# Kernel tuning notes

Measured on AMD Instinct MI355X. Metric: run time of the kernel, lower is better.

Reference implementation:

```python
import jax, jax.numpy as jnp
import numpy as np

N, H, V, K = 2048, 1024, 50304, 16
C = V // K  # tokens per POS cluster


def setup_inputs() -> dict:
    key = jax.random.key(0)
    kx, ky, kw, kl = jax.random.split(key, 4)
    x = jax.random.normal(kx, (N, H), dtype=jnp.float32)
    y = jax.random.randint(ky, (N,), 0, V, dtype=jnp.int32)
    # consistent POS label: token y belongs to cluster y // C
    y_pos = (y // C).astype(jnp.int32)
    # pos2token[i] = token ids of cluster i (equal contiguous partition)
    pos2token = jnp.arange(V, dtype=jnp.int32).reshape(K, C)
    # token_in_pos_id[i][v] = within-cluster index of token v in cluster i
    token_in_pos_id = jnp.broadcast_to(jnp.arange(V, dtype=jnp.int32) % C, (K, V))
    cluster_w = jax.random.normal(kw, (H, K), dtype=jnp.float32) * 0.02
    logits = jax.random.normal(kl, (H, V), dtype=jnp.float32) * 0.02
    return {"x": x, "y": y, "y_pos": y_pos, "pos2token": pos2token,
            "token_in_pos_id": token_in_pos_id, "cluster_w": cluster_w, "logits": logits}


def reference(x, y, y_pos, pos2token, token_in_pos_id, cluster_w, logits):
    # cluster (POS) log-probs: [N, K]
    cluster_ll = jax.nn.log_softmax(x @ cluster_w, axis=1)
    # per-cluster weight slices gathered once: [H, K, C]
    W = logits[:, pos2token.reshape(-1)].reshape(H, K, C)
    # tail logits for every token against every cluster's token set: [N, K, C]
    tail_lp = jax.nn.log_softmax(jnp.einsum('nh,hkc->nkc', x, W), axis=-1)
    n = jnp.arange(y.shape[0])
    within = token_in_pos_id[y_pos, y]          # within-cluster target id
    nll = -cluster_ll[n, y_pos] - tail_lp[n, y_pos, within]
    return nll
```

## Files before the change

kernel.cpp:

```cpp
#include <hip/hip_runtime.h>
#include <hip/hip_bf16.h>
#include <stdint.h>

#define NROW 2048
#define HDIM 1024
#define VOC  50304
#define KCL  16
#define CDIM 3144

#define MT 64
#define NT 256
#define BK 32
#define PK 36
#define NCT 13
#define MAXTILES 48

#define WS_SUMEXP 0
#define WS_COUNTS 2048
#define WS_PART   2064
#define WS_ZTGT   4112
#define WS_TCOL   6160
#define WS_ROWS   8208
#define WS_NTILE  40976
#define WS_TILES  40977

typedef unsigned short u16;
typedef __attribute__((ext_vector_type(8))) short short8;
typedef __attribute__((ext_vector_type(4))) short short4v;
typedef __attribute__((ext_vector_type(4))) float f32x4;
typedef __attribute__((ext_vector_type(4))) unsigned short ushort4v;

__device__ __forceinline__ ushort2 f2bf2(float a, float b) {
    union { __hip_bfloat162 h; ushort2 u; } cv;
    cv.h = __float22bfloat162_rn(float2{a, b});
    return cv.u;
}

__global__ void scatter_kernel(const int* __restrict__ y,
                               const int* __restrict__ y_pos,
                               const int* __restrict__ tip,
                               int* ws_i) {
    int n = blockIdx.x * 256 + threadIdx.x;
    if (n >= NROW) return;
    int kn = y_pos[n];
    int slot = atomicAdd(&ws_i[WS_COUNTS + kn], 1);
    ws_i[WS_ROWS + kn * NROW + slot] = n;
    ws_i[WS_TCOL + n] = tip[kn * VOC + y[n]];
}

__global__ void plan_kernel(int* ws_i) {
    int lane = threadIdx.x;
    int nt = (lane < KCL) ? (ws_i[WS_COUNTS + lane] + MT - 1) / MT : 0;
    int pre = nt;
#pragma unroll
    for (int off = 1; off < 16; off <<= 1) {
        int v = __shfl_up(pre, off);
        if ((lane & 15) >= off) pre += v;
    }
    int start = pre - nt;
    if (lane < KCL) {
        for (int r = 0; r < nt; r++) {
            ws_i[WS_TILES + 2 * (start + r)]     = lane;
            ws_i[WS_TILES + 2 * (start + r) + 1] = r;
        }
        if (lane == KCL - 1) ws_i[WS_NTILE] = start + nt;
    }
}

__global__ void cluster_kernel(const float* __restrict__ x,
                               const float* __restrict__ cw,
                               const int* __restrict__ y_pos,
                               float* ws_f) {
    int wave = threadIdx.x >> 6;
    int lane = threadIdx.x & 63;
    int n = blockIdx.x * 4 + wave;
    float acc[KCL];
#pragma unroll
    for (int k = 0; k < KCL; k++) acc[k] = 0.f;
#pragma unroll
    for (int j = 0; j < 16; j++) {
        int h = j * 64 + lane;
        float xv = x[(size_t)n * HDIM + h];
        const float4* cwr = (const float4*)(cw + (size_t)h * KCL);
#pragma unroll
        for (int q = 0; q < 4; q++) {
            float4 w = cwr[q];
            acc[q * 4 + 0] += xv * w.x;
            acc[q * 4 + 1] += xv * w.y;
            acc[q * 4 + 2] += xv * w.z;
            acc[q * 4 + 3] += xv * w.w;
        }
    }
#pragma unroll
    for (int off = 32; off >= 1; off >>= 1) {
#pragma unroll
        for (int k = 0; k < KCL; k++) acc[k] += __shfl_down(acc[k], off);
    }
    if (lane == 0) {
        int kn = y_pos[n];
        float m = acc[0];
#pragma unroll
        for (int k = 1; k < KCL; k++) m = fmaxf(m, acc[k]);
        float s = 0.f, skn = 0.f;
#pragma unroll
        for (int k = 0; k < KCL; k++) {
            s += __expf(acc[k] - m);
            skn = (k == kn) ? acc[k] : skn;
        }
        ws_f[WS_PART + n] = (m + __logf(s)) - skn;
    }
}

__launch_bounds__(256)
__global__ void tail_kernel(const float* __restrict__ x,
                            const float* __restrict__ logits,
                            const int* ws_i, float* ws_f) {
    __shared__ __align__(16) u16 As[MT * PK];
    __shared__ __align__(16) u16 Bs[NT * PK];
    __shared__ int   lrow[MT];
    __shared__ int   ltcol[MT];
    __shared__ float rowsum[MT];

    const int ntile = ws_i[WS_NTILE];
    if ((int)blockIdx.y >= ntile) return;
    const int kcl = ws_i[WS_TILES + 2 * blockIdx.y];
    const int rt  = ws_i[WS_TILES + 2 * blockIdx.y + 1];
    const int ct  = blockIdx.x;
    const int Mk  = ws_i[WS_COUNTS + kcl];

    const int tid = threadIdx.x;
    if (tid < MT) {
        int r = rt * MT + tid;
        int rid = (r < Mk) ? ws_i[WS_ROWS + kcl * NROW + r] : -1;
        lrow[tid]  = rid;
        ltcol[tid] = (rid >= 0) ? ws_i[WS_TCOL + rid] : -1;
        rowsum[tid] = 0.f;
    }
    __syncthreads();

    const int w    = tid >> 6;
    const int l    = tid & 63;
    const int quad = l >> 4;
    const int lm   = l & 15;

    const int arow = tid >> 2;
    const int ak0  = (tid & 3) * 8;
    int rid_s = lrow[arow]; if (rid_s < 0) rid_s = 0;
    const float* ap = x + (size_t)rid_s * HDIM + ak0;
    int gc = ct * NT + tid; if (gc >= CDIM) gc = CDIM - 1;
    const float* bp = logits + (size_t)(kcl * CDIM + gc);

    float ar[8];
    float br[BK];
#pragma unroll
    for (int j = 0; j < 8; j++) ar[j] = ap[j];
#pragma unroll
    for (int k = 0; k < BK; k++) br[k] = bp[(size_t)k * VOC];
    ap += BK;
    bp += (size_t)BK * VOC;

    f32x4 acc[4][4];
#pragma unroll
    for (int mi = 0; mi < 4; mi++)
#pragma unroll
        for (int ni = 0; ni < 4; ni++) acc[mi][ni] = (f32x4)(0.f);

    union fr { short4v h[2]; short8 s; };

    for (int h0 = 0; h0 < HDIM; h0 += BK) {
#pragma unroll
        for (int jj = 0; jj < 2; jj++) {
            ushort2 p0 = f2bf2(ar[jj * 4 + 0], ar[jj * 4 + 1]);
            ushort2 p1 = f2bf2(ar[jj * 4 + 2], ar[jj * 4 + 3]);
            ushort4v v = {p0.x, p0.y, p1.x, p1.y};
            *(ushort4v*)&As[arow * PK + ak0 + jj * 4] = v;
        }
#pragma unroll
        for (int j = 0; j < 8; j++) {
            ushort2 p0 = f2bf2(br[j * 4 + 0], br[j * 4 + 1]);
            ushort2 p1 = f2bf2(br[j * 4 + 2], br[j * 4 + 3]);
            ushort4v v = {p0.x, p0.y, p1.x, p1.y};
            *(ushort4v*)&Bs[tid * PK + j * 4] = v;
        }
        __syncthreads();

        if (h0 + BK < HDIM) {
#pragma unroll
            for (int j = 0; j < 8; j++) ar[j] = ap[j];
#pragma unroll
            for (int k = 0; k < BK; k++) br[k] = bp[(size_t)k * VOC];
            ap += BK;
            bp += (size_t)BK * VOC;
        }

        short8 a[4], b[4];
#pragma unroll
        for (int mi = 0; mi < 4; mi++) {
            fr f;
            const short4v* p = (const short4v*)&As[(mi * 16 + lm) * PK + quad * 8];
            f.h[0] = p[0]; f.h[1] = p[1];
            a[mi] = f.s;
        }
#pragma unroll
        for (int ni = 0; ni < 4; ni++) {
            fr f;
            const short4v* p = (const short4v*)&Bs[(w * 64 + ni * 16 + lm) * PK + quad * 8];
            f.h[0] = p[0]; f.h[1] = p[1];
            b[ni] = f.s;
        }
#pragma unroll
        for (int mi = 0; mi < 4; mi++)
#pragma unroll
            for (int ni = 0; ni < 4; ni++)
                acc[mi][ni] = __builtin_amdgcn_mfma_f32_16x16x32_bf16(
                    a[mi], b[ni], acc[mi][ni], 0, 0, 0);
        __syncthreads();
    }

#pragma unroll
    for (int mi = 0; mi < 4; mi++) {
#pragma unroll
        for (int r = 0; r < 4; r++) {
            int row_local = mi * 16 + quad * 4 + r;
            int rid = lrow[row_local];
            int tc  = ltcol[row_local];
            float s = 0.f;
#pragma unroll
            for (int ni = 0; ni < 4; ni++) {
                int cl = ct * NT + w * 64 + ni * 16 + lm;
                float z = acc[mi][ni][r];
                if (rid >= 0 && cl < CDIM) {
                    s += __expf(z);
                    if (cl == tc) ws_f[WS_ZTGT + rid] = z;
                }
            }
            s += __shfl_xor(s, 1);
            s += __shfl_xor(s, 2);
            s += __shfl_xor(s, 4);
            s += __shfl_xor(s, 8);
            if (lm == 0 && rid >= 0) atomicAdd(&rowsum[row_local], s);
        }
    }
    __syncthreads();
    if (tid < MT) {
        int rid = lrow[tid];
        if (rid >= 0) atomicAdd(&ws_f[WS_SUMEXP + rid], rowsum[tid]);
    }
}

__global__ void finalize_kernel(const float* ws_f, float* __restrict__ out) {
    int n = blockIdx.x * 256 + threadIdx.x;
    if (n >= NROW) return;
    out[n] = ws_f[WS_PART + n] + __logf(ws_f[WS_SUMEXP + n]) - ws_f[WS_ZTGT + n];
}

extern "C" void kernel_launch(void* const* d_in, const int* in_sizes, int n_in,
                              void* d_out, int out_size, void* d_ws, size_t ws_size,
                              hipStream_t stream) {
    const float* x      = (const float*)d_in[0];
    const int*   y      = (const int*)d_in[1];
    const int*   y_pos  = (const int*)d_in[2];
    const int*   tip    = (const int*)d_in[4];
    const float* cw     = (const float*)d_in[5];
    const float* logits = (const float*)d_in[6];
    float* out  = (float*)d_out;
    float* ws_f = (float*)d_ws;
    int*   ws_i = (int*)d_ws;

    hipMemsetAsync(d_ws, 0, (size_t)(NROW + KCL) * 4, stream);

    scatter_kernel<<<NROW / 256, 256, 0, stream>>>(y, y_pos, tip, ws_i);
    plan_kernel<<<1, 64, 0, stream>>>(ws_i);
    cluster_kernel<<<NROW / 4, 256, 0, stream>>>(x, cw, y_pos, ws_f);

    dim3 grid(NCT, MAXTILES);
    tail_kernel<<<grid, 256, 0, stream>>>(x, logits, ws_i, ws_f);

    finalize_kernel<<<NROW / 256, 256, 0, stream>>>(ws_f, out);
}
```

Baseline: 345.4 us.

## Reshape tail GEMM tiles to 128x128 and pre-convert x to bf16 with direct LDS loads

Switches the tail GEMM tile from 64 rows x 256 columns to 128x128 and arranges the four waves in a 2x2 layout. With about 128 rows per cluster, each cluster's logits columns should now be re-read for fewer row tiles. A new kernel converts x to bf16 in workspace once, so the A operand can be fetched with global_load_lds straight into an unpadded LDS tile. The cost is an extra kernel launch, a 4 MB workspace buffer, and wasted work in a mostly empty second row tile when a cluster has more than 128 rows. The unpadded A tile may also cause LDS bank conflicts.

```diff
diff --git a/kernel.cpp b/kernel.cpp
--- a/kernel.cpp
+++ b/kernel.cpp
@@ -8,12 +8,12 @@
 #define KCL  16
 #define CDIM 3144
 
-#define MT 64
-#define NT 256
+#define MT 128
+#define NT 128
 #define BK 32
 #define PK 36
-#define NCT 13
-#define MAXTILES 48
+#define NCT 25
+#define MAXTILES 32
 
 #define WS_SUMEXP 0
 #define WS_COUNTS 2048
@@ -23,6 +23,7 @@
 #define WS_ROWS   8208
 #define WS_NTILE  40976
 #define WS_TILES  40977
+#define WS_XB     65536
 
 typedef unsigned short u16;
 typedef __attribute__((ext_vector_type(8))) short short8;
@@ -34,6 +35,12 @@
     union { __hip_bfloat162 h; ushort2 u; } cv;
     cv.h = __float22bfloat162_rn(float2{a, b});
     return cv.u;
+}
+
+__device__ __forceinline__ void gload16(const void* g, void* lds) {
+    __builtin_amdgcn_global_load_lds(
+        (__attribute__((address_space(1))) void*)(g),
+        (__attribute__((address_space(3))) void*)(lds), 16, 0, 0);
 }
 
 __global__ void scatter_kernel(const int* __restrict__ y,
@@ -111,11 +118,20 @@
     }
 }
 
+__global__ void convx_kernel(const float* __restrict__ x, u16* __restrict__ xb) {
+    int t = blockIdx.x * 256 + threadIdx.x;
+    float4 f = ((const float4*)x)[t];
+    ushort2 a = f2bf2(f.x, f.y);
+    ushort2 b = f2bf2(f.z, f.w);
+    ushort4v v = {a.x, a.y, b.x, b.y};
+    *(ushort4v*)(xb + (size_t)t * 4) = v;
+}
+
 __launch_bounds__(256)
-__global__ void tail_kernel(const float* __restrict__ x,
+__global__ void tail_kernel(const u16* __restrict__ xb,
                             const float* __restrict__ logits,
                             const int* ws_i, float* ws_f) {
-    __shared__ __align__(16) u16 As[MT * PK];
+    __shared__ __align__(16) u16 As[MT * BK];
     __shared__ __align__(16) u16 Bs[NT * PK];
     __shared__ int   lrow[MT];
     __shared__ int   ltcol[MT];
@@ -143,20 +159,23 @@
     const int quad = l >> 4;
     const int lm   = l & 15;
 
-    const int arow = tid >> 2;
-    const int ak0  = (tid & 3) * 8;
-    int rid_s = lrow[arow]; if (rid_s < 0) rid_s = 0;
-    const float* ap = x + (size_t)rid_s * HDIM + ak0;
-    int gc = ct * NT + tid; if (gc >= CDIM) gc = CDIM - 1;
-    const float* bp = logits + (size_t)(kcl * CDIM + gc);
-
-    float ar[8];
-    float br[BK];
-#pragma unroll
-    for (int j = 0; j < 8; j++) ar[j] = ap[j];
-#pragma unroll
-    for (int k = 0; k < BK; k++) br[k] = bp[(size_t)k * VOC];
-    ap += BK;
+    int ar0 = w * 32 + (l >> 2);
+    int ar1 = ar0 + 16;
+    int rid0 = lrow[ar0]; if (rid0 < 0) rid0 = 0;
+    int rid1 = lrow[ar1]; if (rid1 < 0) rid1 = 0;
+    const u16* agp0 = xb + (size_t)rid0 * HDIM + (l & 3) * 8;
+    const u16* agp1 = xb + (size_t)rid1 * HDIM + (l & 3) * 8;
+    char* alds0 = (char*)As + w * 2048;
+    char* alds1 = (char*)As + w * 2048 + 1024;
+
+    const int bc  = tid & 127;
+    const int bk0 = (tid >> 7) * 16;
+    int gc = ct * NT + bc; if (gc >= CDIM) gc = CDIM - 1;
+    const float* bp = logits + (size_t)(kcl * CDIM + gc) + (size_t)bk0 * VOC;
+
+    float br[16];
+#pragma unroll
+    for (int k = 0; k < 16; k++) br[k] = bp[(size_t)k * VOC];
     bp += (size_t)BK * VOC;
 
     f32x4 acc[4][4];
@@ -165,46 +184,37 @@
 #pragma unroll
         for (int ni = 0; ni < 4; ni++) acc[mi][ni] = (f32x4)(0.f);
 
+    const int wr = (w >> 1) * 64;
+    const int wc = (w & 1) * 64;
     union fr { short4v h[2]; short8 s; };
 
     for (int h0 = 0; h0 < HDIM; h0 += BK) {
-#pragma unroll
-        for (int jj = 0; jj < 2; jj++) {
-            ushort2 p0 = f2bf2(ar[jj * 4 + 0], ar[jj * 4 + 1]);
-            ushort2 p1 = f2bf2(ar[jj * 4 + 2], ar[jj * 4 + 3]);
-            ushort4v v = {p0.x, p0.y, p1.x, p1.y};
-            *(ushort4v*)&As[arow * PK + ak0 + jj * 4] = v;
-        }
-#pragma unroll
-        for (int j = 0; j < 8; j++) {
+        gload16(agp0, alds0);
+        gload16(agp1, alds1);
+        agp0 += BK; agp1 += BK;
+#pragma unroll
+        for (int j = 0; j < 4; j++) {
             ushort2 p0 = f2bf2(br[j * 4 + 0], br[j * 4 + 1]);
             ushort2 p1 = f2bf2(br[j * 4 + 2], br[j * 4 + 3]);
             ushort4v v = {p0.x, p0.y, p1.x, p1.y};
-            *(ushort4v*)&Bs[tid * PK + j * 4] = v;
+            *(ushort4v*)&Bs[bc * PK + bk0 + j * 4] = v;
         }
         __syncthreads();
 
         if (h0 + BK < HDIM) {
 #pragma unroll
-            for (int j = 0; j < 8; j++) ar[j] = ap[j];
-#pragma unroll
-            for (int k = 0; k < BK; k++) br[k] = bp[(size_t)k * VOC];
-            ap += BK;
+            for (int k = 0; k < 16; k++) br[k] = bp[(size_t)k * VOC];
             bp += (size_t)BK * VOC;
         }
 
         short8 a[4], b[4];
 #pragma unroll
-        for (int mi = 0; mi < 4; mi++) {
-            fr f;
-            const short4v* p = (const short4v*)&As[(mi * 16 + lm) * PK + quad * 8];
-            f.h[0] = p[0]; f.h[1] = p[1];
-            a[mi] = f.s;
-        }
+        for (int mi = 0; mi < 4; mi++)
+            a[mi] = *(const short8*)&As[(wr + mi * 16 + lm) * BK + quad * 8];
 #pragma unroll
         for (int ni = 0; ni < 4; ni++) {
             fr f;
-            const short4v* p = (const short4v*)&Bs[(w * 64 + ni * 16 + lm) * PK + quad * 8];
+            const short4v* p = (const short4v*)&Bs[(wc + ni * 16 + lm) * PK + quad * 8];
             f.h[0] = p[0]; f.h[1] = p[1];
             b[ni] = f.s;
         }
@@ -221,13 +231,13 @@
     for (int mi = 0; mi < 4; mi++) {
 #pragma unroll
         for (int r = 0; r < 4; r++) {
-            int row_local = mi * 16 + quad * 4 + r;
+            int row_local = wr + mi * 16 + quad * 4 + r;
             int rid = lrow[row_local];
             int tc  = ltcol[row_local];
             float s = 0.f;
 #pragma unroll
             for (int ni = 0; ni < 4; ni++) {
-                int cl = ct * NT + w * 64 + ni * 16 + lm;
+                int cl = ct * NT + wc + ni * 16 + lm;
                 float z = acc[mi][ni][r];
                 if (rid >= 0 && cl < CDIM) {
                     s += __expf(z);
@@ -266,15 +276,17 @@
     float* out  = (float*)d_out;
     float* ws_f = (float*)d_ws;
     int*   ws_i = (int*)d_ws;
+    u16*   xb   = (u16*)((float*)d_ws + WS_XB);
 
     hipMemsetAsync(d_ws, 0, (size_t)(NROW + KCL) * 4, stream);
 
     scatter_kernel<<<NROW / 256, 256, 0, stream>>>(y, y_pos, tip, ws_i);
     plan_kernel<<<1, 64, 0, stream>>>(ws_i);
     cluster_kernel<<<NROW / 4, 256, 0, stream>>>(x, cw, y_pos, ws_f);
+    convx_kernel<<<NROW * HDIM / 4 / 256, 256, 0, stream>>>(x, xb);
 
     dim3 grid(NCT, MAXTILES);
-    tail_kernel<<<grid, 256, 0, stream>>>(x, logits, ws_i, ws_f);
+    tail_kernel<<<grid, 256, 0, stream>>>(xb, logits, ws_i, ws_f);
 
     finalize_kernel<<<NROW / 256, 256, 0, stream>>>(ws_f, out);
 }
```

Measured after the change: 346.1 us. About the same (+0.2%).
